# Optimization experiments

Hardware: AMD Instinct MI355X
Metric: run time of the kernel (lower is better)

Reference implementation:

```python
import jax, jax.numpy as jnp
import numpy as np
import math

D_MODEL = 1024
N_HEADS = 16
D_HEAD = D_MODEL // N_HEADS
NUM_BUCKETS = 32
MAX_DISTANCE = 128
B, LQ, LK = 2, 2048, 2048


def _rel_pos_bucket(rel):
    # rel: [Lq, Lk] int32, rel = mem - ctx
    n = jnp.clip(-rel, 0, None)
    max_exact = NUM_BUCKETS // 2
    is_small = n < max_exact
    val_if_large = max_exact + (
        jnp.log(n.astype(jnp.float32) / max_exact + 1e-9)
        / math.log(MAX_DISTANCE / max_exact)
        * (NUM_BUCKETS - max_exact)
    ).astype(jnp.int32)
    val_if_large = jnp.minimum(val_if_large, NUM_BUCKETS - 1)
    return jnp.where(is_small, n, val_if_large)


def setup_inputs() -> dict:
    key = jax.random.key(0)
    ks = jax.random.split(key, 9)
    scale = 1.0 / math.sqrt(D_MODEL)
    q = jax.random.normal(ks[0], (B, LQ, D_MODEL), dtype=jnp.float32)
    k = jax.random.normal(ks[1], (B, LK, D_MODEL), dtype=jnp.float32)
    v = jax.random.normal(ks[2], (B, LK, D_MODEL), dtype=jnp.float32)
    key_padding_mask = jax.random.randint(ks[3], (B, 1, 1, LK), 0, 2).astype(bool)
    Wq = jax.random.normal(ks[4], (D_MODEL, D_MODEL), dtype=jnp.float32) * scale
    Wk = jax.random.normal(ks[5], (D_MODEL, D_MODEL), dtype=jnp.float32) * scale
    Wv = jax.random.normal(ks[6], (D_MODEL, D_MODEL), dtype=jnp.float32) * scale
    Wo = jax.random.normal(ks[7], (D_MODEL, D_MODEL), dtype=jnp.float32) * scale
    rel_emb = jax.random.normal(ks[8], (NUM_BUCKETS, N_HEADS), dtype=jnp.float32) * 0.02
    return {"q": q, "k": k, "v": v, "key_padding_mask": key_padding_mask,
            "Wq": Wq, "Wk": Wk, "Wv": Wv, "Wo": Wo, "rel_emb": rel_emb}


def reference(q, k, v, key_padding_mask, Wq, Wk, Wv, Wo, rel_emb):
    Bq, Lq, _ = q.shape
    Lk = k.shape[1]
    # projections (nn.Linear: x @ W.T), split heads -> [B, H, L, dh]
    qh = (q @ Wq.T).reshape(Bq, Lq, N_HEADS, D_HEAD).transpose(0, 2, 1, 3)
    kh = (k @ Wk.T).reshape(Bq, Lk, N_HEADS, D_HEAD).transpose(0, 2, 1, 3)
    vh = (v @ Wv.T).reshape(Bq, Lk, N_HEADS, D_HEAD).transpose(0, 2, 1, 3)
    scores = jnp.einsum('bhqd,bhkd->bhqk', qh, kh) / math.sqrt(D_HEAD)
    # relative position bias: [1, H, Lq, Lk]
    rel = jnp.arange(Lk, dtype=jnp.int32)[None, :] - jnp.arange(Lq, dtype=jnp.int32)[:, None]
    buckets = _rel_pos_bucket(rel)  # [Lq, Lk]
    bias = rel_emb[buckets]         # [Lq, Lk, H]
    scores = scores + bias.transpose(2, 0, 1)[None]
    scores = jnp.where(key_padding_mask, scores, -1e9)
    attn = jax.nn.softmax(scores, axis=-1)
    out = jnp.einsum('bhqk,bhkd->bhqd', attn, vh)
    out = out.transpose(0, 2, 1, 3).reshape(Bq, Lq, D_MODEL)
    return out @ Wo.T
```

## Files before the change

### kernel.cpp

```cpp
#include <hip/hip_runtime.h>
#include <math.h>

typedef _Float16 f16;
typedef __fp16 h16x2 __attribute__((ext_vector_type(2)));
typedef _Float16 f16x4 __attribute__((ext_vector_type(4)));
typedef _Float16 f16x8 __attribute__((ext_vector_type(8)));
typedef float f32x4 __attribute__((ext_vector_type(4)));
typedef float f32x16 __attribute__((ext_vector_type(16)));
typedef unsigned int u32;

#define D_MODEL 1024
#define NHEADS 16
#define DHEAD 64
#define LQ 2048
#define LKK 2048
#define BB 2
#define LOG2E 1.4426950408889634f

static __device__ __forceinline__ void gload16(const void* g, void* l) {
  __builtin_amdgcn_global_load_lds(
      (const __attribute__((address_space(1))) u32*)g,
      (__attribute__((address_space(3))) u32*)l, 16, 0, 0);
}
static __device__ __forceinline__ float ex2(float x) {
  float r;
  asm volatile("v_exp_f32 %0, %1\n\ts_nop 0" : "=v"(r) : "v"(x));
  return r;
}
static __device__ __forceinline__ u32 pkr(float a, float b) {
  union { h16x2 h; u32 u; } c;
  c.h = __builtin_amdgcn_cvt_pkrtz(a, b);
  return c.u;
}
static __device__ __forceinline__ float fmax3(float a, float b, float c) {
  return fmaxf(fmaxf(a, b), c);
}
#define MFMA16(a, b, c) __builtin_amdgcn_mfma_f32_16x16x32_f16(a, b, c, 0, 0, 0)
#define MFMA32(a, b, c) __builtin_amdgcn_mfma_f32_32x32x16_f16(a, b, c, 0, 0, 0)

__global__ void k_cvtw_prep(const float* Wq, const float* Wk, const float* Wv, const float* Wo,
                            f16* W16, const void* msk, const float* __restrict__ rel,
                            float* __restrict__ biasT, unsigned char* __restrict__ m8) {
  const int blk = blockIdx.x;
  const int t = threadIdx.x;
  if (blk < 4096) {
    int i = blk * 256 + t;
    int which = i >> 18, off = i & 262143;
    const float* s = which == 0 ? Wq : (which == 1 ? Wk : (which == 2 ? Wv : Wo));
    float4 x = ((const float4*)s)[off];
    f16x4 o; o[0] = (f16)x.x; o[1] = (f16)x.y; o[2] = (f16)x.z; o[3] = (f16)x.w;
    ((f16x4*)(W16 + (size_t)which * 1048576))[off] = o;
    return;
  }
  if (blk == 4096) {
    __shared__ int o1s, o2s;
    if (t == 0) { o1s = 0; o2s = 0; }
    __syncthreads();
    const unsigned char* raw = (const unsigned char*)msk;
    int o1 = 0, o2 = 0;
    for (int i = t; i < BB * LKK; i += 256) {
      unsigned char vv = raw[i];
      if ((i & 3) && vv) o1 = 1;
      if (((i & 3) == 2) && vv == 0x80u) o2 = 1;
    }
    if (o1) atomicOr(&o1s, 1);
    if (o2) atomicOr(&o2s, 1);
    __syncthreads();
    const int f = o1s ? (o2s ? 2 : 1) : 0;
    for (int i = t; i < BB * LKK; i += 256) {
      unsigned char vv;
      if (f == 0)      vv = (((const int*)msk)[i] != 0);
      else if (f == 1) vv = (((const unsigned char*)msk)[i] != 0);
      else             vv = (((const float*)msk)[i] != 0.0f);
      m8[i] = vv;
    }
    return;
  }
  for (int n = t; n < 2048; n += 256) {
    int bucket;
    if (n < 16) bucket = n;
    else {
      float tt = logf((float)n / 16.0f + 1e-9f);
      tt = tt / 2.0794415416798357f;
      tt = tt * 16.0f;
      bucket = 16 + (int)tt;
      if (bucket > 31) bucket = 31;
    }
    for (int h = 0; h < NHEADS; ++h)
      biasT[h * 2048 + n] = rel[bucket * NHEADS + h] * LOG2E;
  }
}

template <int EPI, int BN, bool AF32>
static __device__ __forceinline__ void gemm_core(const void* __restrict__ Av,
                                                 const f16* __restrict__ Bm,
                                                 void* __restrict__ C,
                                                 f16* sA, f16* sB) {
  constexpr int JN = BN / 32;
  const int t = threadIdx.x;
  const int w = t >> 6, lane = t & 63;
  const int lg = lane >> 4, lc = lane & 15;
  const int wr = w >> 1, wc = w & 1;
  const long row0 = (long)blockIdx.x * 128;
  const long col0 = (long)blockIdx.y * BN;
  f32x4 acc[4][JN] = {};

  const int rA0 = t >> 2, kA0 = t & 3;
  const int rA1 = (t + 256) >> 2;

  float4 a[4];

  auto LOADA = [&](int kk) {
    const float* s0 = (const float*)Av + (row0 + rA0) * 1024 + kk * 32 + kA0 * 8;
    const float* s1 = (const float*)Av + (row0 + rA1) * 1024 + kk * 32 + kA0 * 8;
    a[0] = *(const float4*)s0; a[1] = *(const float4*)(s0 + 4);
    a[2] = *(const float4*)s1; a[3] = *(const float4*)(s1 + 4);
  };
  auto WRITEA = [&](int buf) {
    f16x8 o0, o1;
    o0[0] = (f16)a[0].x; o0[1] = (f16)a[0].y; o0[2] = (f16)a[0].z; o0[3] = (f16)a[0].w;
    o0[4] = (f16)a[1].x; o0[5] = (f16)a[1].y; o0[6] = (f16)a[1].z; o0[7] = (f16)a[1].w;
    o1[0] = (f16)a[2].x; o1[1] = (f16)a[2].y; o1[2] = (f16)a[2].z; o1[3] = (f16)a[2].w;
    o1[4] = (f16)a[3].x; o1[5] = (f16)a[3].y; o1[6] = (f16)a[3].z; o1[7] = (f16)a[3].w;
    *(f16x8*)((char*)sA + buf * 8192 + t * 16) = o0;
    *(f16x8*)((char*)sA + buf * 8192 + (t + 256) * 16) = o1;
  };
  auto STAGEA16 = [&](int kk, int buf) {
    gload16((const f16*)Av + (row0 + rA0) * 1024 + kk * 32 + kA0 * 8,
            (char*)sA + buf * 8192 + t * 16);
    gload16((const f16*)Av + (row0 + rA1) * 1024 + kk * 32 + kA0 * 8,
            (char*)sA + buf * 8192 + (t + 256) * 16);
  };
  auto STAGEB = [&](int kk, int buf) {
#pragma unroll
    for (int it = 0; it < BN / 64; ++it) {
      int ch = t + it * 256;
      int r = ch >> 2, kq = ch & 3;
      gload16(Bm + (col0 + r) * 1024 + kk * 32 + kq * 8, (char*)sB + buf * BN * 64 + ch * 16);
    }
  };
  auto COMPUTE = [&](int buf) {
    f16x8 af[4], bf[JN];
#pragma unroll
    for (int i = 0; i < 4; ++i)
      af[i] = *(const f16x8*)&sA[buf * 4096 + (wr * 64 + i * 16 + lc) * 32 + lg * 8];
#pragma unroll
    for (int j = 0; j < JN; ++j)
      bf[j] = *(const f16x8*)&sB[buf * BN * 32 + (wc * (16 * JN) + j * 16 + lc) * 32 + lg * 8];
#pragma unroll
    for (int i = 0; i < 4; ++i)
#pragma unroll
      for (int j = 0; j < JN; ++j)
        acc[i][j] = MFMA16(af[i], bf[j], acc[i][j]);
  };

  if constexpr (AF32) { LOADA(0); WRITEA(0); } else { STAGEA16(0, 0); }
  STAGEB(0, 0);
  __syncthreads();

  for (int kk = 0; kk < 32; ++kk) {
    const int cur = kk & 1;
    if (kk < 31) {
      if constexpr (AF32) { LOADA(kk + 1); } else { STAGEA16(kk + 1, cur ^ 1); }
      STAGEB(kk + 1, cur ^ 1);
    }
    COMPUTE(cur);
    if (kk < 31) { if constexpr (AF32) WRITEA(cur ^ 1); }
    __syncthreads();
  }

#pragma unroll
  for (int i = 0; i < 4; ++i)
#pragma unroll
    for (int j = 0; j < JN; ++j) {
      const long rowb = row0 + wr * 64 + i * 16 + lg * 4;
      const long col = col0 + wc * (16 * JN) + j * 16 + lc;
      if (EPI == 2) {
        long b = rowb >> 11, l0 = rowb & 2047;
        long h = col >> 6, d = col & 63;
        f16x4 ov;
#pragma unroll
        for (int r = 0; r < 4; ++r) ov[r] = (f16)acc[i][j][r];
        *(f16x4*)((f16*)C + (((b * NHEADS + h) * DHEAD + d) * (long)LKK + l0)) = ov;
      } else {
#pragma unroll
        for (int r = 0; r < 4; ++r) {
          long row = rowb + r;
          float vv = acc[i][j][r];
          if (EPI == 0) {
            long b = row >> 11, l = row & 2047;
            long h = col >> 6, d = col & 63;
            ((f16*)C)[(((b * NHEADS + h) * LQ) + l) * DHEAD + d] = (f16)vv;
          } else {
            ((float*)C)[row * 1024 + col] = vv;
          }
        }
      }
    }
}

__global__ void __launch_bounds__(256, 3)
k_gemm_qkv(const float* __restrict__ q, const float* __restrict__ k, const float* __restrict__ v,
           const f16* __restrict__ W16, f16* __restrict__ QHp, f16* __restrict__ KHp,
           f16* __restrict__ VTp) {
  __shared__ __align__(16) f16 smem[16384];
  f16* sA = smem;
  f16* sB = smem + 8192;
  const int z = blockIdx.z;
  if (z == 2) {
    gemm_core<2, 128, true>(v, W16 + 2 * 1048576, VTp, sA, sB);
  } else {
    const float* A = z == 0 ? q : k;
    f16* C = z == 0 ? QHp : KHp;
    gemm_core<0, 128, true>(A, W16 + (size_t)z * 1048576, C, sA, sB);
  }
}

__global__ void __launch_bounds__(256, 2)
k_gemm_o(const f16* __restrict__ A, const f16* __restrict__ Bm, float* __restrict__ C) {
  __shared__ __align__(16) f16 smem[2 * 4096 + 2 * 2048];
  gemm_core<1, 64, false>(A, Bm, C, smem, smem + 8192);
}

__global__ void __launch_bounds__(256, 4)
k_attn(const f16* __restrict__ QH, const f16* __restrict__ KH, const f16* __restrict__ VT,
       const float* __restrict__ BIASg, const unsigned char* __restrict__ M8,
       f16* __restrict__ OUT) {
  constexpr int KR = LKK;
  constexpr int NT = KR / 64;
  __shared__ __align__(16) f16 sK[2][64 * 64];
  __shared__ __align__(16) f16 sVT[2][64 * 64];
  __shared__ __align__(16) float sBias[KR + 128];
  __shared__ __align__(16) f16 sPen[KR + 8];

  const int L = blockIdx.x;
  const int bh = (L & 7) * 4 + ((L >> 3) & 3);
  const int qc = (L >> 5) & 15;
  const int b = bh >> 4, h = bh & 15;
  const int t = threadIdx.x, w = t >> 6, lane = t & 63;
  const int lq = lane & 31, hi = lane >> 5;
  const int q0 = qc * 128;
  const int q0w = q0 + w * 32;
  const size_t base = (size_t)bh * LKK * DHEAD;

  for (int i = t; i < KR + 128; i += 256) {
    int n = i - (KR - 1) + q0;
    n = n < 0 ? 0 : (n > 2047 ? 2047 : n);
    sBias[i] = BIASg[h * 2048 + n];
  }
  for (int i = t; i < KR; i += 256)
    sPen[i] = M8[b * LKK + i] ? (f16)0.0f : (f16)-60000.0f;

  f16x8 qb[4];
  const f16* qrow = QH + base + (size_t)(q0w + lq) * DHEAD;
#pragma unroll
  for (int s = 0; s < 4; ++s)
    qb[s] = *(const f16x8*)(qrow + s * 16 + hi * 8);

  const int ch0 = t, ch1 = t + 256;
  const int r0 = ch0 >> 3, g0 = ((ch0 & 7) ^ (r0 & 7)) * 8;
  const int r1 = ch1 >> 3, g1 = ((ch1 & 7) ^ (r1 & 7)) * 8;
  const f16* Kb = KH + base;
  const f16* Vb = VT + base;

  auto STAGE = [&](int kt, int buf) {
    const int k0 = kt * 64;
    gload16(Kb + (size_t)(k0 + r0) * DHEAD + g0, (char*)&sK[buf][0] + ch0 * 16);
    gload16(Kb + (size_t)(k0 + r1) * DHEAD + g1, (char*)&sK[buf][0] + ch1 * 16);
    gload16(Vb + (size_t)r0 * LKK + k0 + g0, (char*)&sVT[buf][0] + ch0 * 16);
    gload16(Vb + (size_t)r1 * LKK + k0 + g1, (char*)&sVT[buf][0] + ch1 * 16);
  };

  float m_r = -1e30f;
  f32x16 oacc0 = {}, oacc1 = {}, oaccL = {};
  const float c1 = 0.125f * LOG2E;
  f16x8 ones;
#pragma unroll
  for (int e = 0; e < 8; ++e) ones[e] = (f16)1.0f;

  STAGE(0, 0);
  __syncthreads();

  for (int it = 0; it < NT; ++it) {
    const int cur = it & 1;
    if (it + 1 < NT) STAGE(it + 1, cur ^ 1);

    const char* sKb = (const char*)&sK[cur][0];
    f32x16 sa0 = {}, sa1 = {};
    __builtin_amdgcn_s_setprio(1);
#pragma unroll
    for (int s = 0; s < 4; ++s) {
      f16x8 k0 = *(const f16x8*)(sKb + ((lq * 128 + s * 32 + hi * 16) ^ ((lq & 7) << 4)));
      f16x8 k1 = *(const f16x8*)(sKb + (((32 + lq) * 128 + s * 32 + hi * 16) ^ ((lq & 7) << 4)));
      sa0 = MFMA32(k0, qb[s], sa0);
      sa1 = MFMA32(k1, qb[s], sa1);
    }
    __builtin_amdgcn_s_setprio(0);

    float p_[32];
#pragma unroll
    for (int r = 0; r < 16; ++r) { p_[r] = sa0[r]; p_[16 + r] = sa1[r]; }

#pragma unroll
    for (int u = 0; u < 8; ++u) {
      int tt = u >> 2, j = u & 3;
      int kloc = it * 64 + tt * 32 + j * 8 + hi * 4;
      f16x4 pen4 = *(const f16x4*)&sPen[kloc];
      int bidx0 = w * 32 + lq - kloc + (KR - 1);
#pragma unroll
      for (int e = 0; e < 4; ++e) {
        float bp = sBias[bidx0 - e] + (float)pen4[e];
        int r = tt * 16 + j * 4 + e;
        p_[r] = p_[r] * c1 + bp;
      }
    }

    float mm[11];
#pragma unroll
    for (int r = 0; r < 10; ++r) mm[r] = fmax3(p_[3 * r], p_[3 * r + 1], p_[3 * r + 2]);
    mm[10] = fmaxf(p_[30], p_[31]);
    float a0 = fmax3(mm[0], mm[1], mm[2]);
    float a1 = fmax3(mm[3], mm[4], mm[5]);
    float a2 = fmax3(mm[6], mm[7], mm[8]);
    float a3 = fmax3(mm[9], mm[10], a0);
    float mx = fmax3(a1, a2, a3);
    mx = fmaxf(mx, __shfl_xor(mx, 32));

    if (__any(mx > m_r + 8.0f)) {
      float mnew = fmaxf(m_r, mx);
      float al = ex2(m_r - mnew);
      m_r = mnew;
#pragma unroll
      for (int r = 0; r < 16; ++r) { oacc0[r] *= al; oacc1[r] *= al; oaccL[r] *= al; }
    }

#pragma unroll
    for (int r = 0; r < 32; ++r) p_[r] = ex2(p_[r] - m_r);

    f16x8 pf[4];
#pragma unroll
    for (int sl = 0; sl < 4; ++sl) {
      int tt = sl >> 1, sp = sl & 1;
      int bA = tt * 16 + (2 * sp) * 4, bB = tt * 16 + (2 * sp + 1) * 4;
      u32 A0 = pkr(p_[bA], p_[bA + 1]);
      u32 A1 = pkr(p_[bA + 2], p_[bA + 3]);
      u32 B0 = pkr(p_[bB], p_[bB + 1]);
      u32 B1 = pkr(p_[bB + 2], p_[bB + 3]);
      asm volatile("v_permlane32_swap_b32 %0, %1" : "+v"(A0), "+v"(B0));
      asm volatile("v_permlane32_swap_b32 %0, %1" : "+v"(A1), "+v"(B1));
      union { u32 u[4]; f16x8 v; } c;
      c.u[0] = A0; c.u[1] = A1; c.u[2] = B0; c.u[3] = B1;
      pf[sl] = c.v;
    }

    const char* sVb = (const char*)&sVT[cur][0];
    __builtin_amdgcn_s_setprio(1);
#pragma unroll
    for (int sl = 0; sl < 4; ++sl) {
      int K0 = sl * 16;
      f16x8 v0 = *(const f16x8*)(sVb + ((lq * 128 + K0 * 2 + hi * 16) ^ ((lq & 7) << 4)));
      f16x8 v1 = *(const f16x8*)(sVb + (((32 + lq) * 128 + K0 * 2 + hi * 16) ^ ((lq & 7) << 4)));
      oacc0 = MFMA32(v0, pf[sl], oacc0);
      oacc1 = MFMA32(v1, pf[sl], oacc1);
      oaccL = MFMA32(ones, pf[sl], oaccL);
    }
    __builtin_amdgcn_s_setprio(0);
    __syncthreads();
  }

  const float l = oaccL[0];
  const float rinv = l > 0.0f ? 1.0f / l : 0.0f;
  const size_t orow = ((size_t)b * LQ + (q0w + lq)) * D_MODEL + h * DHEAD;
#pragma unroll
  for (int dh = 0; dh < 2; ++dh)
#pragma unroll
    for (int j = 0; j < 4; ++j) {
      int d0 = dh * 32 + j * 8 + hi * 4;
      f16x4 ov;
#pragma unroll
      for (int e = 0; e < 4; ++e)
        ov[e] = (f16)((dh ? oacc1[j * 4 + e] : oacc0[j * 4 + e]) * rinv);
      *(f16x4*)(OUT + orow + d0) = ov;
    }
}

extern "C" void kernel_launch(void* const* d_in, const int* in_sizes, int n_in,
                              void* d_out, int out_size, void* d_ws, size_t ws_size,
                              hipStream_t stream) {
  (void)in_sizes; (void)n_in; (void)out_size; (void)ws_size;
  const float* q   = (const float*)d_in[0];
  const float* k   = (const float*)d_in[1];
  const float* v   = (const float*)d_in[2];
  const void*  msk = d_in[3];
  const float* Wq  = (const float*)d_in[4];
  const float* Wk  = (const float*)d_in[5];
  const float* Wv  = (const float*)d_in[6];
  const float* Wo  = (const float*)d_in[7];
  const float* rel = (const float*)d_in[8];

  char* ws = (char*)d_ws;
  const size_t SL = (size_t)8 << 20;
  f16* QHp = (f16*)(ws + 0 * SL);
  f16* KHp = (f16*)(ws + 1 * SL);
  f16* VTp = (f16*)(ws + 2 * SL);
  f16* O16 = (f16*)(ws + 3 * SL);
  f16* W16 = (f16*)(ws + 4 * SL);
  char* misc = ws + 5 * SL;
  float* BIAS = (float*)misc;
  unsigned char* M8 = (unsigned char*)(misc + (192 << 10));

  k_cvtw_prep<<<4098, 256, 0, stream>>>(Wq, Wk, Wv, Wo, W16, msk, rel, BIAS, M8);
  k_gemm_qkv<<<dim3(32, 8, 3), 256, 0, stream>>>(q, k, v, W16, QHp, KHp, VTp);
  k_attn<<<512, 256, 0, stream>>>(QHp, KHp, VTp, BIAS, M8, O16);
  k_gemm_o<<<dim3(32, 16), 256, 0, stream>>>(O16, W16 + 3 * 1048576, (float*)d_out);
}
```

Measured before the change: 149.5 us.

## Restore older attention kernel variant with full-range bias table and fp32 penalties

The attention kernel goes back to an earlier shape. Launch bounds drop from 4 to 2 waves per SIMD, the s_setprio hints around the MFMA blocks are removed, and the bias table now covers the full relative-position range instead of a per-query-chunk window. The key-padding penalty is stored as fp32 (-3e9) instead of fp16, and the zero-denominator guard on the final normalisation is removed. This increases LDS use (larger bias table, float penalty array) and may lower occupancy, while removing a little per-block index arithmetic.

```diff
diff --git a/kernel.cpp b/kernel.cpp
--- a/kernel.cpp
+++ b/kernel.cpp
@@ -222,34 +222,30 @@
   gemm_core<1, 64, false>(A, Bm, C, smem, smem + 8192);
 }
 
-__global__ void __launch_bounds__(256, 4)
+__global__ void __launch_bounds__(256, 2)
 k_attn(const f16* __restrict__ QH, const f16* __restrict__ KH, const f16* __restrict__ VT,
        const float* __restrict__ BIASg, const unsigned char* __restrict__ M8,
-       f16* __restrict__ OUT) {
-  constexpr int KR = LKK;
-  constexpr int NT = KR / 64;
+       f16* __restrict__ O16) {
   __shared__ __align__(16) f16 sK[2][64 * 64];
   __shared__ __align__(16) f16 sVT[2][64 * 64];
-  __shared__ __align__(16) float sBias[KR + 128];
-  __shared__ __align__(16) f16 sPen[KR + 8];
+  __shared__ __align__(16) float sBias[4104];
+  __shared__ __align__(16) float sPen[2048];
 
   const int L = blockIdx.x;
   const int bh = (L & 7) * 4 + ((L >> 3) & 3);
-  const int qc = (L >> 5) & 15;
+  const int qc = L >> 5;
   const int b = bh >> 4, h = bh & 15;
   const int t = threadIdx.x, w = t >> 6, lane = t & 63;
   const int lq = lane & 31, hi = lane >> 5;
-  const int q0 = qc * 128;
-  const int q0w = q0 + w * 32;
+  const int q0w = qc * 128 + w * 32;
   const size_t base = (size_t)bh * LKK * DHEAD;
 
-  for (int i = t; i < KR + 128; i += 256) {
-    int n = i - (KR - 1) + q0;
-    n = n < 0 ? 0 : (n > 2047 ? 2047 : n);
+  for (int i = t; i < 4104; i += 256) {
+    int n = i - 2052; n = n < 0 ? 0 : (n > 2047 ? 2047 : n);
     sBias[i] = BIASg[h * 2048 + n];
   }
-  for (int i = t; i < KR; i += 256)
-    sPen[i] = M8[b * LKK + i] ? (f16)0.0f : (f16)-60000.0f;
+  for (int i = t; i < 2048; i += 256)
+    sPen[i] = M8[b * LKK + i] ? 0.0f : -3.0e9f;
 
   f16x8 qb[4];
   const f16* qrow = QH + base + (size_t)(q0w + lq) * DHEAD;
@@ -281,13 +277,12 @@
   STAGE(0, 0);
   __syncthreads();
 
-  for (int it = 0; it < NT; ++it) {
-    const int cur = it & 1;
-    if (it + 1 < NT) STAGE(it + 1, cur ^ 1);
+  for (int kt = 0; kt < 32; ++kt) {
+    const int cur = kt & 1;
+    if (kt < 31) STAGE(kt + 1, cur ^ 1);
 
     const char* sKb = (const char*)&sK[cur][0];
     f32x16 sa0 = {}, sa1 = {};
-    __builtin_amdgcn_s_setprio(1);
 #pragma unroll
     for (int s = 0; s < 4; ++s) {
       f16x8 k0 = *(const f16x8*)(sKb + ((lq * 128 + s * 32 + hi * 16) ^ ((lq & 7) << 4)));
@@ -295,7 +290,6 @@
       sa0 = MFMA32(k0, qb[s], sa0);
       sa1 = MFMA32(k1, qb[s], sa1);
     }
-    __builtin_amdgcn_s_setprio(0);
 
     float p_[32];
 #pragma unroll
@@ -304,12 +298,12 @@
 #pragma unroll
     for (int u = 0; u < 8; ++u) {
       int tt = u >> 2, j = u & 3;
-      int kloc = it * 64 + tt * 32 + j * 8 + hi * 4;
-      f16x4 pen4 = *(const f16x4*)&sPen[kloc];
-      int bidx0 = w * 32 + lq - kloc + (KR - 1);
+      int kbase = kt * 64 + tt * 32 + j * 8 + hi * 4;
+      f32x4 pen4 = *(const f32x4*)&sPen[kbase];
+      int bidx0 = (q0w + lq) - kbase + 2052;
 #pragma unroll
       for (int e = 0; e < 4; ++e) {
-        float bp = sBias[bidx0 - e] + (float)pen4[e];
+        float bp = sBias[bidx0 - e] + pen4[e];
         int r = tt * 16 + j * 4 + e;
         p_[r] = p_[r] * c1 + bp;
       }
@@ -354,7 +348,6 @@
     }
 
     const char* sVb = (const char*)&sVT[cur][0];
-    __builtin_amdgcn_s_setprio(1);
 #pragma unroll
     for (int sl = 0; sl < 4; ++sl) {
       int K0 = sl * 16;
@@ -364,12 +357,10 @@
       oacc1 = MFMA32(v1, pf[sl], oacc1);
       oaccL = MFMA32(ones, pf[sl], oaccL);
     }
-    __builtin_amdgcn_s_setprio(0);
     __syncthreads();
   }
 
-  const float l = oaccL[0];
-  const float rinv = l > 0.0f ? 1.0f / l : 0.0f;
+  const float rinv = 1.0f / oaccL[0];
   const size_t orow = ((size_t)b * LQ + (q0w + lq)) * D_MODEL + h * DHEAD;
 #pragma unroll
   for (int dh = 0; dh < 2; ++dh)
@@ -378,9 +369,11 @@
       int d0 = dh * 32 + j * 8 + hi * 4;
       f16x4 ov;
 #pragma unroll
-      for (int e = 0; e < 4; ++e)
-        ov[e] = (f16)((dh ? oacc1[j * 4 + e] : oacc0[j * 4 + e]) * rinv);
-      *(f16x4*)(OUT + orow + d0) = ov;
+      for (int e = 0; e < 4; ++e) {
+        float x = (dh ? oacc1[j * 4 + e] : oacc0[j * 4 + e]) * rinv;
+        ov[e] = (f16)x;
+      }
+      *(f16x4*)(O16 + orow + d0) = ov;
     }
 }
 
```

Measured after the change: 142.3 us. -4.8%, faster.
